# Kernel optimization log

Measured on AMD Instinct MI355X. Metric: run time of the kernel, lower is better.

Reference implementation:

```python
import jax, jax.numpy as jnp
import numpy as np

DIM = 512

def setup_inputs() -> dict:
    key = jax.random.key(0)
    k1, k2, k3 = jax.random.split(key, 3)
    context = jax.random.normal(k1, (64, 1024, DIM), dtype=jnp.float32)
    query = jax.random.normal(k2, (64, 128, DIM), dtype=jnp.float32)
    # nn.Linear(3*dim, 1, bias=False) weight, flattened to a (3*dim,) vector
    w0 = jax.random.normal(k3, (3 * DIM,), dtype=jnp.float32) * (1.0 / np.sqrt(3 * DIM))
    return {"context": context, "query": query, "w0": w0}

def reference(context, query, w0):
    # Trilinear similarity: sim[b,i,j] = w_c.c_i + w_q.q_j + w_m.(c_i*q_j)
    # (equivalent to Linear(concat([c, q, c*q])) without materializing the concat)
    d = context.shape[-1]
    wc, wq, wm = w0[:d], w0[d:2 * d], w0[2 * d:]
    sim = (context @ wc)[:, :, None] \
        + (query @ wq)[:, None, :] \
        + jnp.einsum('bid,bjd->bij', context * wm, query)  # (B, ctx, q)
    # Original: softmax over trailing dim of size 1 -> all ones (faithful to the bug)
    S = jnp.ones_like(sim)                 # (B, ctx, q)
    SS = jax.nn.softmax(sim, axis=1)       # softmax over context dim
    A = S @ query                          # (B, ctx, d)
    B = S @ jnp.swapaxes(SS, 1, 2) @ context  # (B, ctx, d)
    return (A, B)
```

## Files before the change

### kernel.cpp

```cpp
#include <hip/hip_runtime.h>
#include <hip/hip_bf16.h>

#define NB   64
#define NC   1024
#define NQ   128
#define DIMD 512
#define BK   64
#define NKC  (DIMD / BK)
#define LDK  (BK + 8)
#define TM   128
#define NTILE (NC / TM)

using short8  = __attribute__((ext_vector_type(8))) short;
using short4v = __attribute__((ext_vector_type(4))) short;
using f32x4   = __attribute__((ext_vector_type(4))) float;
typedef __fp16 half2v __attribute__((ext_vector_type(2)));

__device__ inline float dot4(float4 a, float4 b) {
    return a.x * b.x + a.y * b.y + a.z * b.z + a.w * b.w;
}

__global__ __launch_bounds__(256) void gemm_stats(
    const float* __restrict__ ctx, const float* __restrict__ qry,
    const float* __restrict__ w0, float* __restrict__ stats,
    unsigned short* __restrict__ simh)
{
    __shared__ __attribute__((aligned(16))) short As[TM][LDK];
    __shared__ __attribute__((aligned(16))) short Bs[NQ][LDK];
    __shared__ __attribute__((aligned(16))) float w0L[3 * DIMD];
    __shared__ float cwL[TM], qwL[NQ];
    __shared__ float sL[2][NQ];

    const int tid  = threadIdx.x;
    const int b    = blockIdx.x;
    const int bt   = blockIdx.y;
    const int i0   = bt * TM;
    const int w    = tid >> 6;
    const int lane = tid & 63;
    const int wr   = w >> 1, wcg = w & 1;
    const int RB   = wr * 64, CB = wcg * 64;
    const int n16  = lane & 15, qd = lane >> 4;

    for (int idx = tid; idx < 3 * DIMD; idx += 256) w0L[idx] = w0[idx];

    f32x4 acc[4][4];
#pragma unroll
    for (int ri = 0; ri < 4; ri++)
#pragma unroll
        for (int ci = 0; ci < 4; ci++)
#pragma unroll
            for (int e = 0; e < 4; e++) acc[ri][ci][e] = 0.f;

    const int col4  = n16 * 4;
    const int srow0 = w * 32 + qd;
    const float* cBase = ctx + ((size_t)(b * NC + i0 + srow0)) * DIMD + col4;
    const float* qBase = qry + ((size_t)(b * NQ + srow0)) * DIMD + col4;
    float cwp[8], qwp[8];
#pragma unroll
    for (int u = 0; u < 8; u++) { cwp[u] = 0.f; qwp[u] = 0.f; }

    for (int kc = 0; kc < NKC; kc++) {
        const int k0 = kc * BK;
        __syncthreads();
        float4 wcv = *(const float4*)&w0L[k0 + col4];
        float4 wqv = *(const float4*)&w0L[DIMD + k0 + col4];
        float4 wmv = *(const float4*)&w0L[2 * DIMD + k0 + col4];
#pragma unroll
        for (int u = 0; u < 8; u++) {
            const int row = w * 32 + u * 4 + qd;
            float4 v = *(const float4*)(cBase + k0 + (size_t)u * 4 * DIMD);
            cwp[u] += dot4(v, wcv);
            union { __hip_bfloat162 h[2]; short4v s; } pc;
            pc.h[0] = __float22bfloat162_rn(make_float2(v.x * wmv.x, v.y * wmv.y));
            pc.h[1] = __float22bfloat162_rn(make_float2(v.z * wmv.z, v.w * wmv.w));
            *(short4v*)&As[row][col4] = pc.s;

            float4 q = *(const float4*)(qBase + k0 + (size_t)u * 4 * DIMD);
            qwp[u] += dot4(q, wqv);
            union { __hip_bfloat162 h[2]; short4v s; } pq;
            pq.h[0] = __float22bfloat162_rn(make_float2(q.x, q.y));
            pq.h[1] = __float22bfloat162_rn(make_float2(q.z, q.w));
            *(short4v*)&Bs[row][col4] = pq.s;
        }
        __syncthreads();
#pragma unroll
        for (int ks = 0; ks < BK / 32; ks++) {
            const int kb = ks * 32 + qd * 8;
            short8 af[4], bfr[4];
#pragma unroll
            for (int ri = 0; ri < 4; ri++) af[ri] = *(const short8*)&As[RB + ri * 16 + n16][kb];
#pragma unroll
            for (int ci = 0; ci < 4; ci++) bfr[ci] = *(const short8*)&Bs[CB + ci * 16 + n16][kb];
#pragma unroll
            for (int ri = 0; ri < 4; ri++)
#pragma unroll
                for (int ci = 0; ci < 4; ci++)
                    acc[ri][ci] = __builtin_amdgcn_mfma_f32_16x16x32_bf16(
                        af[ri], bfr[ci], acc[ri][ci], 0, 0, 0);
        }
    }

#pragma unroll
    for (int u = 0; u < 8; u++) {
        float c = cwp[u], q = qwp[u];
#pragma unroll
        for (int off = 1; off < 16; off <<= 1) {
            c += __shfl_xor(c, off);
            q += __shfl_xor(q, off);
        }
        if (n16 == 0) {
            const int row = w * 32 + u * 4 + qd;
            cwL[row] = c; qwL[row] = q;
        }
    }
    __syncthreads();

#pragma unroll
    for (int ci = 0; ci < 4; ci++) {
        const int col = CB + ci * 16 + n16;
        const float qwv = qwL[col];
        unsigned short* simCol = simh + ((size_t)(b * NTILE + bt) * NQ + col) * TM;
        float s = 0.f;
#pragma unroll
        for (int ri = 0; ri < 4; ri++) {
            const int rbase = RB + ri * 16 + qd * 4;
            float v0 = acc[ri][ci][0] + cwL[rbase + 0] + qwv;
            float v1 = acc[ri][ci][1] + cwL[rbase + 1] + qwv;
            float v2 = acc[ri][ci][2] + cwL[rbase + 2] + qwv;
            float v3 = acc[ri][ci][3] + cwL[rbase + 3] + qwv;
            s += __expf(v0) + __expf(v1) + __expf(v2) + __expf(v3);
            half2v h01 = __builtin_amdgcn_cvt_pkrtz(v0, v1);
            half2v h23 = __builtin_amdgcn_cvt_pkrtz(v2, v3);
            uint2 pk;
            pk.x = __builtin_bit_cast(unsigned, h01);
            pk.y = __builtin_bit_cast(unsigned, h23);
            *(uint2*)&simCol[rbase] = pk;
        }
        s += __shfl_xor(s, 16);
        s += __shfl_xor(s, 32);
        if (qd == 0) sL[wr][col] = s;
    }
    __syncthreads();
    if (tid < NQ)
        stats[(size_t)(b * NTILE + bt) * NQ + tid] = sL[0][tid] + sL[1][tid];
}

__global__ void combine_stats(const float* __restrict__ stats, float* __restrict__ colstats)
{
    const int b = blockIdx.x, j = threadIdx.x;
    float s = 0.f;
    for (int t = 0; t < NTILE; t++)
        s += stats[(size_t)(b * NTILE + t) * NQ + j];
    colstats[(size_t)b * NQ + j] = 1.0f / s;
}

__global__ void arow_kernel(const float* __restrict__ qry, float* __restrict__ arow)
{
    const int b = blockIdx.x, h = blockIdx.y;
    const int d = h * 256 + threadIdx.x;
    float a = 0.f;
    const float* base = qry + (size_t)b * NQ * DIMD + d;
    for (int j = 0; j < NQ; j++) a += base[(size_t)j * DIMD];
    arow[(size_t)b * DIMD + d] = a;
}

__global__ __launch_bounds__(256) void rb_kernel(
    const float* __restrict__ ctx, const unsigned short* __restrict__ simh,
    const float* __restrict__ colstats, float* __restrict__ bpart)
{
    __shared__ __attribute__((aligned(16))) unsigned short simL[NQ * TM];
    __shared__ float izL[NQ];
    __shared__ float rpart[2][TM];
    __shared__ float rfin[TM];

    const int tid = threadIdx.x;
    const int b = blockIdx.x, bt = blockIdx.y;
    const int i0 = bt * TM;

    if (tid < NQ) izL[tid] = colstats[(size_t)b * NQ + tid];
    const unsigned short* tileSrc = simh + (size_t)(b * NTILE + bt) * NQ * TM;
#pragma unroll
    for (int it = 0; it < 8; it++) {
        const int idx = (tid + it * 256) * 8;
        *(uint4*)&simL[idx] = *(const uint4*)&tileSrc[idx];
    }
    __syncthreads();

    const int i = tid & 127, jh = tid >> 7;
    float r = 0.f;
    for (int j2 = 0; j2 < 64; j2++) {
        const int j = jh * 64 + j2;
        __fp16 hv = __builtin_bit_cast(__fp16, simL[j * TM + i]);
        r += __expf((float)hv) * izL[j];
    }
    rpart[jh][i] = r;
    __syncthreads();
    if (tid < TM) rfin[tid] = rpart[0][tid] + rpart[1][tid];
    __syncthreads();

    const int d0 = tid * 2;
    float bx = 0.f, by = 0.f;
    const float* cb2 = ctx + ((size_t)b * NC + i0) * DIMD + d0;
    for (int ii = 0; ii < TM; ii++) {
        float  rv = rfin[ii];
        float2 cv = *(const float2*)(cb2 + (size_t)ii * DIMD);
        bx += rv * cv.x; by += rv * cv.y;
    }
    float* bp = bpart + (size_t)(b * NTILE + bt) * DIMD + d0;
    bp[0] = bx; bp[1] = by;
}

__global__ void broadcast_out(const float* __restrict__ arow, const float* __restrict__ bpart,
                              float* __restrict__ out)
{
    const int b = blockIdx.x, ic = blockIdx.y;
    const int t = threadIdx.x;
    const int half = t >> 7;
    const int l = t & 127;
    const int d0 = l * 4;
    float4 val;
    if (half == 0) {
        val = *(const float4*)&arow[(size_t)b * DIMD + d0];
    } else {
        val.x = val.y = val.z = val.w = 0.f;
        for (int t8 = 0; t8 < NTILE; t8++) {
            float4 v = *(const float4*)&bpart[(size_t)(b * NTILE + t8) * DIMD + d0];
            val.x += v.x; val.y += v.y; val.z += v.z; val.w += v.w;
        }
    }
    size_t base = (size_t)half * ((size_t)NB * NC * DIMD)
                + ((size_t)b * NC + (size_t)ic * 32) * DIMD + d0;
    for (int i = 0; i < 32; i++)
        *(float4*)&out[base + (size_t)i * DIMD] = val;
}

extern "C" void kernel_launch(void* const* d_in, const int* in_sizes, int n_in,
                              void* d_out, int out_size, void* d_ws, size_t ws_size,
                              hipStream_t stream)
{
    const float* ctx = (const float*)d_in[0];
    const float* qry = (const float*)d_in[1];
    const float* w0  = (const float*)d_in[2];
    float* out = (float*)d_out;
    float* ws  = (float*)d_ws;

    float* stats    = ws;
    float* colstats = ws + 65536;
    float* arow     = ws + 73728;
    float* bpart    = ws + 106496;
    unsigned short* simh = (unsigned short*)(ws + 524288);

    arow_kernel<<<dim3(NB, 2), 256, 0, stream>>>(qry, arow);
    gemm_stats<<<dim3(NB, NTILE), 256, 0, stream>>>(ctx, qry, w0, stats, simh);
    combine_stats<<<NB, NQ, 0, stream>>>(stats, colstats);
    rb_kernel<<<dim3(NB, NTILE), 256, 0, stream>>>(ctx, simh, colstats, bpart);
    broadcast_out<<<dim3(NB, 32), 256, 0, stream>>>(arow, bpart, out);
}
```

Before: 432.1 us.

## Precompute bf16 operands and row dots in a prep kernel; async LDS loads in GEMM

Adds a prep kernel that converts context to bf16 and the weighted query to bf16, and computes the per-row context and query linear terms once. The GEMM then streams pre-converted bf16 tiles into swizzled LDS via global_load_lds and reads B fragments directly from global memory, removing in-loop conversion and weight application. The column-sum combine kernel is folded into rb_kernel, and rb_kernel reads bf16 context instead of fp32. This adds an extra pass over context and lowers the precision of the B output path.

```diff
diff --git a/kernel.cpp b/kernel.cpp
--- a/kernel.cpp
+++ b/kernel.cpp
@@ -7,29 +7,85 @@
 #define DIMD 512
 #define BK   64
 #define NKC  (DIMD / BK)
-#define LDK  (BK + 8)
 #define TM   128
 #define NTILE (NC / TM)
 
 using short8  = __attribute__((ext_vector_type(8))) short;
-using short4v = __attribute__((ext_vector_type(4))) short;
 using f32x4   = __attribute__((ext_vector_type(4))) float;
 typedef __fp16 half2v __attribute__((ext_vector_type(2)));
 
 __device__ inline float dot4(float4 a, float4 b) {
     return a.x * b.x + a.y * b.y + a.z * b.z + a.w * b.w;
 }
+__device__ inline float bf2f(unsigned short u) {
+    unsigned x = ((unsigned)u) << 16;
+    return __builtin_bit_cast(float, x);
+}
+__device__ inline ushort2 pkbf(float a, float b) {
+    union { __hip_bfloat162 h; ushort2 u; } x;
+    x.h = __float22bfloat162_rn(make_float2(a, b));
+    return x.u;
+}
+#define GLOAD_LDS16(g, l)                                             \
+    __builtin_amdgcn_global_load_lds(                                 \
+        (const __attribute__((address_space(1))) void*)(g),           \
+        (__attribute__((address_space(3))) void*)(l), 16, 0, 0)
+
+__global__ __launch_bounds__(256) void prep_kernel(
+    const float* __restrict__ ctx, const float* __restrict__ qry,
+    const float* __restrict__ w0,
+    unsigned short* __restrict__ C2, unsigned short* __restrict__ Q2,
+    float* __restrict__ cwG, float* __restrict__ qwG)
+{
+    const int wv   = blockIdx.x * 4 + (threadIdx.x >> 6);
+    const int lane = threadIdx.x & 63;
+    const int c0 = lane * 4, c1 = 256 + lane * 4;
+
+    if (wv < NB * NC) {
+        const float* src = ctx + (size_t)wv * DIMD;
+        float4 v0 = *(const float4*)(src + c0);
+        float4 v1 = *(const float4*)(src + c1);
+        float4 w0v = *(const float4*)(w0 + c0);
+        float4 w1v = *(const float4*)(w0 + c1);
+        float d = dot4(v0, w0v) + dot4(v1, w1v);
+#pragma unroll
+        for (int off = 1; off < 64; off <<= 1) d += __shfl_xor(d, off);
+        if (lane == 0) cwG[wv] = d;
+        ushort2 p0 = pkbf(v0.x, v0.y), p1 = pkbf(v0.z, v0.w);
+        ushort2 p2 = pkbf(v1.x, v1.y), p3 = pkbf(v1.z, v1.w);
+        union { ushort2 u2[2]; uint2 u; } a, bb;
+        a.u2[0] = p0; a.u2[1] = p1; bb.u2[0] = p2; bb.u2[1] = p3;
+        *(uint2*)&C2[(size_t)wv * DIMD + c0] = a.u;
+        *(uint2*)&C2[(size_t)wv * DIMD + c1] = bb.u;
+    } else {
+        const int r2 = wv - NB * NC;
+        const float* src = qry + (size_t)r2 * DIMD;
+        float4 v0 = *(const float4*)(src + c0);
+        float4 v1 = *(const float4*)(src + c1);
+        float4 wq0 = *(const float4*)(w0 + DIMD + c0);
+        float4 wq1 = *(const float4*)(w0 + DIMD + c1);
+        float4 wm0 = *(const float4*)(w0 + 2 * DIMD + c0);
+        float4 wm1 = *(const float4*)(w0 + 2 * DIMD + c1);
+        float d = dot4(v0, wq0) + dot4(v1, wq1);
+#pragma unroll
+        for (int off = 1; off < 64; off <<= 1) d += __shfl_xor(d, off);
+        if (lane == 0) qwG[r2] = d;
+        ushort2 p0 = pkbf(v0.x * wm0.x, v0.y * wm0.y), p1 = pkbf(v0.z * wm0.z, v0.w * wm0.w);
+        ushort2 p2 = pkbf(v1.x * wm1.x, v1.y * wm1.y), p3 = pkbf(v1.z * wm1.z, v1.w * wm1.w);
+        union { ushort2 u2[2]; uint2 u; } a, bb;
+        a.u2[0] = p0; a.u2[1] = p1; bb.u2[0] = p2; bb.u2[1] = p3;
+        *(uint2*)&Q2[(size_t)r2 * DIMD + c0] = a.u;
+        *(uint2*)&Q2[(size_t)r2 * DIMD + c1] = bb.u;
+    }
+}
 
 __global__ __launch_bounds__(256) void gemm_stats(
-    const float* __restrict__ ctx, const float* __restrict__ qry,
-    const float* __restrict__ w0, float* __restrict__ stats,
-    unsigned short* __restrict__ simh)
-{
-    __shared__ __attribute__((aligned(16))) short As[TM][LDK];
-    __shared__ __attribute__((aligned(16))) short Bs[NQ][LDK];
-    __shared__ __attribute__((aligned(16))) float w0L[3 * DIMD];
-    __shared__ float cwL[TM], qwL[NQ];
-    __shared__ float sL[2][NQ];
+    const unsigned short* __restrict__ C2, const unsigned short* __restrict__ Q2,
+    const float* __restrict__ cwG, const float* __restrict__ qwG,
+    float* __restrict__ stats, unsigned short* __restrict__ simh)
+{
+    __shared__ __attribute__((aligned(16))) unsigned short As[TM * BK];
+    __shared__ float cwL[TM], qwL[NQ], sL[2][NQ];
 
     const int tid  = threadIdx.x;
     const int b    = blockIdx.x;
@@ -41,7 +97,8 @@
     const int RB   = wr * 64, CB = wcg * 64;
     const int n16  = lane & 15, qd = lane >> 4;
 
-    for (int idx = tid; idx < 3 * DIMD; idx += 256) w0L[idx] = w0[idx];
+    if (tid < TM) cwL[tid] = cwG[b * NC + i0 + tid];
+    if (tid < NQ) qwL[tid] = qwG[b * NQ + tid];
 
     f32x4 acc[4][4];
 #pragma unroll
@@ -51,46 +108,30 @@
 #pragma unroll
             for (int e = 0; e < 4; e++) acc[ri][ci][e] = 0.f;
 
-    const int col4  = n16 * 4;
-    const int srow0 = w * 32 + qd;
-    const float* cBase = ctx + ((size_t)(b * NC + i0 + srow0)) * DIMD + col4;
-    const float* qBase = qry + ((size_t)(b * NQ + srow0)) * DIMD + col4;
-    float cwp[8], qwp[8];
-#pragma unroll
-    for (int u = 0; u < 8; u++) { cwp[u] = 0.f; qwp[u] = 0.f; }
+    const int a8 = lane >> 3, p8 = lane & 7;
+    const int kgd = p8 ^ (a8 & 7);
+    const unsigned short* gA = C2 + ((size_t)(b * NC + i0 + w * 32 + a8)) * DIMD + kgd * 8;
+    unsigned short* ldsA = &As[(w * 32) * BK];
+    const int sw = n16 & 7;
 
     for (int kc = 0; kc < NKC; kc++) {
         const int k0 = kc * BK;
         __syncthreads();
-        float4 wcv = *(const float4*)&w0L[k0 + col4];
-        float4 wqv = *(const float4*)&w0L[DIMD + k0 + col4];
-        float4 wmv = *(const float4*)&w0L[2 * DIMD + k0 + col4];
-#pragma unroll
-        for (int u = 0; u < 8; u++) {
-            const int row = w * 32 + u * 4 + qd;
-            float4 v = *(const float4*)(cBase + k0 + (size_t)u * 4 * DIMD);
-            cwp[u] += dot4(v, wcv);
-            union { __hip_bfloat162 h[2]; short4v s; } pc;
-            pc.h[0] = __float22bfloat162_rn(make_float2(v.x * wmv.x, v.y * wmv.y));
-            pc.h[1] = __float22bfloat162_rn(make_float2(v.z * wmv.z, v.w * wmv.w));
-            *(short4v*)&As[row][col4] = pc.s;
-
-            float4 q = *(const float4*)(qBase + k0 + (size_t)u * 4 * DIMD);
-            qwp[u] += dot4(q, wqv);
-            union { __hip_bfloat162 h[2]; short4v s; } pq;
-            pq.h[0] = __float22bfloat162_rn(make_float2(q.x, q.y));
-            pq.h[1] = __float22bfloat162_rn(make_float2(q.z, q.w));
-            *(short4v*)&Bs[row][col4] = pq.s;
-        }
+#pragma unroll
+        for (int u = 0; u < 4; u++)
+            GLOAD_LDS16(gA + k0 + (size_t)u * 8 * DIMD, ldsA + u * 8 * BK);
         __syncthreads();
 #pragma unroll
-        for (int ks = 0; ks < BK / 32; ks++) {
-            const int kb = ks * 32 + qd * 8;
+        for (int ks = 0; ks < 2; ks++) {
             short8 af[4], bfr[4];
 #pragma unroll
-            for (int ri = 0; ri < 4; ri++) af[ri] = *(const short8*)&As[RB + ri * 16 + n16][kb];
-#pragma unroll
-            for (int ci = 0; ci < 4; ci++) bfr[ci] = *(const short8*)&Bs[CB + ci * 16 + n16][kb];
+            for (int ci = 0; ci < 4; ci++)
+                bfr[ci] = *(const short8*)(Q2 + ((size_t)(b * NQ + CB + ci * 16 + n16)) * DIMD
+                                           + k0 + ks * 32 + qd * 8);
+#pragma unroll
+            for (int ri = 0; ri < 4; ri++)
+                af[ri] = *(const short8*)&As[(RB + ri * 16 + n16) * BK
+                                             + (((ks * 4 + qd) ^ sw) * 8)];
 #pragma unroll
             for (int ri = 0; ri < 4; ri++)
 #pragma unroll
@@ -99,21 +140,6 @@
                         af[ri], bfr[ci], acc[ri][ci], 0, 0, 0);
         }
     }
-
-#pragma unroll
-    for (int u = 0; u < 8; u++) {
-        float c = cwp[u], q = qwp[u];
-#pragma unroll
-        for (int off = 1; off < 16; off <<= 1) {
-            c += __shfl_xor(c, off);
-            q += __shfl_xor(q, off);
-        }
-        if (n16 == 0) {
-            const int row = w * 32 + u * 4 + qd;
-            cwL[row] = c; qwL[row] = q;
-        }
-    }
-    __syncthreads();
 
 #pragma unroll
     for (int ci = 0; ci < 4; ci++) {
@@ -145,15 +171,6 @@
         stats[(size_t)(b * NTILE + bt) * NQ + tid] = sL[0][tid] + sL[1][tid];
 }
 
-__global__ void combine_stats(const float* __restrict__ stats, float* __restrict__ colstats)
-{
-    const int b = blockIdx.x, j = threadIdx.x;
-    float s = 0.f;
-    for (int t = 0; t < NTILE; t++)
-        s += stats[(size_t)(b * NTILE + t) * NQ + j];
-    colstats[(size_t)b * NQ + j] = 1.0f / s;
-}
-
 __global__ void arow_kernel(const float* __restrict__ qry, float* __restrict__ arow)
 {
     const int b = blockIdx.x, h = blockIdx.y;
@@ -165,8 +182,8 @@
 }
 
 __global__ __launch_bounds__(256) void rb_kernel(
-    const float* __restrict__ ctx, const unsigned short* __restrict__ simh,
-    const float* __restrict__ colstats, float* __restrict__ bpart)
+    const unsigned short* __restrict__ C2, const unsigned short* __restrict__ simh,
+    const float* __restrict__ stats, float* __restrict__ bpart)
 {
     __shared__ __attribute__((aligned(16))) unsigned short simL[NQ * TM];
     __shared__ float izL[NQ];
@@ -177,7 +194,12 @@
     const int b = blockIdx.x, bt = blockIdx.y;
     const int i0 = bt * TM;
 
-    if (tid < NQ) izL[tid] = colstats[(size_t)b * NQ + tid];
+    if (tid < NQ) {
+        float s = 0.f;
+        for (int t = 0; t < NTILE; t++)
+            s += stats[(size_t)(b * NTILE + t) * NQ + tid];
+        izL[tid] = 1.0f / s;
+    }
     const unsigned short* tileSrc = simh + (size_t)(b * NTILE + bt) * NQ * TM;
 #pragma unroll
     for (int it = 0; it < 8; it++) {
@@ -200,11 +222,11 @@
 
     const int d0 = tid * 2;
     float bx = 0.f, by = 0.f;
-    const float* cb2 = ctx + ((size_t)b * NC + i0) * DIMD + d0;
+    const unsigned short* cb2 = C2 + ((size_t)(b * NC + i0)) * DIMD + d0;
     for (int ii = 0; ii < TM; ii++) {
-        float  rv = rfin[ii];
-        float2 cv = *(const float2*)(cb2 + (size_t)ii * DIMD);
-        bx += rv * cv.x; by += rv * cv.y;
+        float rv = rfin[ii];
+        ushort2 cv = *(const ushort2*)(cb2 + (size_t)ii * DIMD);
+        bx += rv * bf2f(cv.x); by += rv * bf2f(cv.y);
     }
     float* bp = bpart + (size_t)(b * NTILE + bt) * DIMD + d0;
     bp[0] = bx; bp[1] = by;
@@ -242,17 +264,20 @@
     const float* qry = (const float*)d_in[1];
     const float* w0  = (const float*)d_in[2];
     float* out = (float*)d_out;
-    float* ws  = (float*)d_ws;
-
-    float* stats    = ws;
-    float* colstats = ws + 65536;
-    float* arow     = ws + 73728;
-    float* bpart    = ws + 106496;
-    unsigned short* simh = (unsigned short*)(ws + 524288);
-
+    char*  ws  = (char*)d_ws;
+
+    float* stats = (float*)(ws);
+    float* arow  = (float*)(ws + (1u << 20));
+    float* bpart = (float*)(ws + (2u << 20));
+    float* cwG   = (float*)(ws + (4u << 20));
+    float* qwG   = (float*)(ws + (5u << 20));
+    unsigned short* simh = (unsigned short*)(ws + (8u << 20));
+    unsigned short* C2   = (unsigned short*)(ws + (32u << 20));
+    unsigned short* Q2   = (unsigned short*)(ws + (104u << 20));
+
+    prep_kernel<<<18432, 256, 0, stream>>>(ctx, qry, w0, C2, Q2, cwG, qwG);
     arow_kernel<<<dim3(NB, 2), 256, 0, stream>>>(qry, arow);
-    gemm_stats<<<dim3(NB, NTILE), 256, 0, stream>>>(ctx, qry, w0, stats, simh);
-    combine_stats<<<NB, NQ, 0, stream>>>(stats, colstats);
-    rb_kernel<<<dim3(NB, NTILE), 256, 0, stream>>>(ctx, simh, colstats, bpart);
+    gemm_stats<<<dim3(NB, NTILE), 256, 0, stream>>>(C2, Q2, cwG, qwG, stats, simh);
+    rb_kernel<<<dim3(NB, NTILE), 256, 0, stream>>>(C2, simh, stats, bpart);
     broadcast_out<<<dim3(NB, 32), 256, 0, stream>>>(arow, bpart, out);
 }
```

Measured after the change: 432.1 us. About the same (+0.0%).

## Fuse column softmax into GEMM by tiling over query columns, drop sim buffer

Applied to the files above, without the earlier changes.

The GEMM is restructured so each block owns 16 query columns across all 1024 context rows. This lets the column softmax normalisation and the row-sum reduction happen in registers, with no fp16 similarity matrix written out and no separate stats-combine pass. The arow reduction is folded into a new brow kernel that also computes the context weighted sum, cutting five launches to three. The trade-off is that context is re-read from global memory by eight blocks per batch (one per query group) and converted to bf16 on the fly. This raises context traffic and reduces per-block MFMA reuse.

```diff
diff --git a/kernel.cpp b/kernel.cpp
--- a/kernel.cpp
+++ b/kernel.cpp
@@ -7,210 +7,187 @@
 #define DIMD 512
 #define BK   64
 #define NKC  (DIMD / BK)
-#define LDK  (BK + 8)
-#define TM   128
-#define NTILE (NC / TM)
+#define LDKB (BK + 8)
 
 using short8  = __attribute__((ext_vector_type(8))) short;
 using short4v = __attribute__((ext_vector_type(4))) short;
 using f32x4   = __attribute__((ext_vector_type(4))) float;
-typedef __fp16 half2v __attribute__((ext_vector_type(2)));
 
 __device__ inline float dot4(float4 a, float4 b) {
     return a.x * b.x + a.y * b.y + a.z * b.z + a.w * b.w;
 }
-
-__global__ __launch_bounds__(256) void gemm_stats(
+__device__ inline short4v pk4(float a, float b, float c, float d) {
+    union { __hip_bfloat162 h[2]; short4v s; } x;
+    x.h[0] = __float22bfloat162_rn(make_float2(a, b));
+    x.h[1] = __float22bfloat162_rn(make_float2(c, d));
+    return x.s;
+}
+
+__global__ __launch_bounds__(256) void colgemm_kernel(
     const float* __restrict__ ctx, const float* __restrict__ qry,
-    const float* __restrict__ w0, float* __restrict__ stats,
-    unsigned short* __restrict__ simh)
-{
-    __shared__ __attribute__((aligned(16))) short As[TM][LDK];
-    __shared__ __attribute__((aligned(16))) short Bs[NQ][LDK];
+    const float* __restrict__ w0, float* __restrict__ rpart)
+{
+    __shared__ __attribute__((aligned(16))) short Bs[16][LDKB];
     __shared__ __attribute__((aligned(16))) float w0L[3 * DIMD];
-    __shared__ float cwL[TM], qwL[NQ];
-    __shared__ float sL[2][NQ];
+    __shared__ float cwL[NC];
+    __shared__ float qwL[16];
+    __shared__ float zL[4][16];
 
     const int tid  = threadIdx.x;
     const int b    = blockIdx.x;
-    const int bt   = blockIdx.y;
-    const int i0   = bt * TM;
+    const int jg   = blockIdx.y;
     const int w    = tid >> 6;
     const int lane = tid & 63;
-    const int wr   = w >> 1, wcg = w & 1;
-    const int RB   = wr * 64, CB = wcg * 64;
     const int n16  = lane & 15, qd = lane >> 4;
 
     for (int idx = tid; idx < 3 * DIMD; idx += 256) w0L[idx] = w0[idx];
 
-    f32x4 acc[4][4];
-#pragma unroll
-    for (int ri = 0; ri < 4; ri++)
-#pragma unroll
-        for (int ci = 0; ci < 4; ci++)
-#pragma unroll
-            for (int e = 0; e < 4; e++) acc[ri][ci][e] = 0.f;
-
-    const int col4  = n16 * 4;
-    const int srow0 = w * 32 + qd;
-    const float* cBase = ctx + ((size_t)(b * NC + i0 + srow0)) * DIMD + col4;
-    const float* qBase = qry + ((size_t)(b * NQ + srow0)) * DIMD + col4;
-    float cwp[8], qwp[8];
-#pragma unroll
-    for (int u = 0; u < 8; u++) { cwp[u] = 0.f; qwp[u] = 0.f; }
+    f32x4 acc[16];
+#pragma unroll
+    for (int rt = 0; rt < 16; rt++)
+#pragma unroll
+        for (int e = 0; e < 4; e++) acc[rt][e] = 0.f;
+
+    const int brow = tid >> 4, bk4 = (tid & 15) * 4;
+    const float* qRow = qry + ((size_t)(b * NQ + jg * 16 + brow)) * DIMD + bk4;
+    float qwp = 0.f;
+
+    const float* cBase = ctx + ((size_t)(b * NC + w * 256 + n16)) * DIMD + qd * 8;
+    float cwp[16];
+#pragma unroll
+    for (int rt = 0; rt < 16; rt++) cwp[rt] = 0.f;
+
+    __syncthreads();
 
     for (int kc = 0; kc < NKC; kc++) {
         const int k0 = kc * BK;
+        {
+            float4 q  = *(const float4*)(qRow + k0);
+            float4 wq = *(const float4*)&w0L[DIMD + k0 + bk4];
+            float4 wm = *(const float4*)&w0L[2 * DIMD + k0 + bk4];
+            qwp += dot4(q, wq);
+            *(short4v*)&Bs[brow][bk4] = pk4(q.x * wm.x, q.y * wm.y, q.z * wm.z, q.w * wm.w);
+        }
         __syncthreads();
-        float4 wcv = *(const float4*)&w0L[k0 + col4];
-        float4 wqv = *(const float4*)&w0L[DIMD + k0 + col4];
-        float4 wmv = *(const float4*)&w0L[2 * DIMD + k0 + col4];
-#pragma unroll
-        for (int u = 0; u < 8; u++) {
-            const int row = w * 32 + u * 4 + qd;
-            float4 v = *(const float4*)(cBase + k0 + (size_t)u * 4 * DIMD);
-            cwp[u] += dot4(v, wcv);
-            union { __hip_bfloat162 h[2]; short4v s; } pc;
-            pc.h[0] = __float22bfloat162_rn(make_float2(v.x * wmv.x, v.y * wmv.y));
-            pc.h[1] = __float22bfloat162_rn(make_float2(v.z * wmv.z, v.w * wmv.w));
-            *(short4v*)&As[row][col4] = pc.s;
-
-            float4 q = *(const float4*)(qBase + k0 + (size_t)u * 4 * DIMD);
-            qwp[u] += dot4(q, wqv);
-            union { __hip_bfloat162 h[2]; short4v s; } pq;
-            pq.h[0] = __float22bfloat162_rn(make_float2(q.x, q.y));
-            pq.h[1] = __float22bfloat162_rn(make_float2(q.z, q.w));
-            *(short4v*)&Bs[row][col4] = pq.s;
+#pragma unroll
+        for (int ks = 0; ks < 2; ks++) {
+            const int kw = k0 + ks * 32 + qd * 8;
+            float4 wc0 = *(const float4*)&w0L[kw];
+            float4 wc1 = *(const float4*)&w0L[kw + 4];
+            short8 bfr = *(const short8*)&Bs[n16][ks * 32 + qd * 8];
+#pragma unroll
+            for (int rt = 0; rt < 16; rt++) {
+                const float* ap = cBase + (size_t)rt * 16 * DIMD + k0 + ks * 32;
+                float4 a0 = *(const float4*)(ap);
+                float4 a1 = *(const float4*)(ap + 4);
+                cwp[rt] += dot4(a0, wc0) + dot4(a1, wc1);
+                union { short4v s4[2]; short8 s8; } af;
+                af.s4[0] = pk4(a0.x, a0.y, a0.z, a0.w);
+                af.s4[1] = pk4(a1.x, a1.y, a1.z, a1.w);
+                acc[rt] = __builtin_amdgcn_mfma_f32_16x16x32_bf16(af.s8, bfr, acc[rt], 0, 0, 0);
+            }
         }
         __syncthreads();
-#pragma unroll
-        for (int ks = 0; ks < BK / 32; ks++) {
-            const int kb = ks * 32 + qd * 8;
-            short8 af[4], bfr[4];
-#pragma unroll
-            for (int ri = 0; ri < 4; ri++) af[ri] = *(const short8*)&As[RB + ri * 16 + n16][kb];
-#pragma unroll
-            for (int ci = 0; ci < 4; ci++) bfr[ci] = *(const short8*)&Bs[CB + ci * 16 + n16][kb];
-#pragma unroll
-            for (int ri = 0; ri < 4; ri++)
-#pragma unroll
-                for (int ci = 0; ci < 4; ci++)
-                    acc[ri][ci] = __builtin_amdgcn_mfma_f32_16x16x32_bf16(
-                        af[ri], bfr[ci], acc[ri][ci], 0, 0, 0);
-        }
-    }
-
-#pragma unroll
-    for (int u = 0; u < 8; u++) {
-        float c = cwp[u], q = qwp[u];
-#pragma unroll
-        for (int off = 1; off < 16; off <<= 1) {
-            c += __shfl_xor(c, off);
-            q += __shfl_xor(q, off);
-        }
-        if (n16 == 0) {
-            const int row = w * 32 + u * 4 + qd;
-            cwL[row] = c; qwL[row] = q;
-        }
-    }
-    __syncthreads();
-
-#pragma unroll
-    for (int ci = 0; ci < 4; ci++) {
-        const int col = CB + ci * 16 + n16;
-        const float qwv = qwL[col];
-        unsigned short* simCol = simh + ((size_t)(b * NTILE + bt) * NQ + col) * TM;
+    }
+
+    {
+        float q = qwp;
+#pragma unroll
+        for (int off = 1; off < 16; off <<= 1) q += __shfl_xor(q, off);
+        if ((tid & 15) == 0 && w == (brow >> 2)) qwL[brow] = q;
+    }
+#pragma unroll
+    for (int rt = 0; rt < 16; rt++) {
+        float c = cwp[rt];
+        c += __shfl_xor(c, 16);
+        c += __shfl_xor(c, 32);
+        if (qd == 0) cwL[w * 256 + rt * 16 + n16] = c;
+    }
+    __syncthreads();
+
+    const float qwv = qwL[n16];
+    float zp = 0.f;
+#pragma unroll
+    for (int rt = 0; rt < 16; rt++) {
+        const int rbase = w * 256 + rt * 16 + qd * 4;
+#pragma unroll
+        for (int rg = 0; rg < 4; rg++) {
+            float e = __expf(acc[rt][rg] + cwL[rbase + rg] + qwv);
+            acc[rt][rg] = e;
+            zp += e;
+        }
+    }
+    zp += __shfl_xor(zp, 16);
+    zp += __shfl_xor(zp, 32);
+    if (qd == 0) zL[w][n16] = zp;
+    __syncthreads();
+    const float iz = 1.0f / (zL[0][n16] + zL[1][n16] + zL[2][n16] + zL[3][n16]);
+
+    float* rp = rpart + ((size_t)(b * 8 + jg)) * NC;
+#pragma unroll
+    for (int rt = 0; rt < 16; rt++) {
+        f32x4 rv;
+#pragma unroll
+        for (int rg = 0; rg < 4; rg++) {
+            float v = acc[rt][rg] * iz;
+#pragma unroll
+            for (int off = 1; off < 16; off <<= 1) v += __shfl_xor(v, off);
+            rv[rg] = v;
+        }
+        if (n16 == 0)
+            *(f32x4*)&rp[w * 256 + rt * 16 + qd * 4] = rv;
+    }
+}
+
+__global__ __launch_bounds__(256) void brow_kernel(
+    const float* __restrict__ ctx, const float* __restrict__ qry,
+    const float* __restrict__ rpart, float* __restrict__ browG,
+    float* __restrict__ arowG)
+{
+    __shared__ float rfullL[NC];
+    __shared__ float bredL[4][64];
+    __shared__ float aredL[4][64];
+
+    const int tid = threadIdx.x;
+    const int b = blockIdx.x, dg = blockIdx.y;
+
+#pragma unroll
+    for (int g = 0; g < 4; g++) {
+        const int i = g * 256 + tid;
         float s = 0.f;
 #pragma unroll
-        for (int ri = 0; ri < 4; ri++) {
-            const int rbase = RB + ri * 16 + qd * 4;
-            float v0 = acc[ri][ci][0] + cwL[rbase + 0] + qwv;
-            float v1 = acc[ri][ci][1] + cwL[rbase + 1] + qwv;
-            float v2 = acc[ri][ci][2] + cwL[rbase + 2] + qwv;
-            float v3 = acc[ri][ci][3] + cwL[rbase + 3] + qwv;
-            s += __expf(v0) + __expf(v1) + __expf(v2) + __expf(v3);
-            half2v h01 = __builtin_amdgcn_cvt_pkrtz(v0, v1);
-            half2v h23 = __builtin_amdgcn_cvt_pkrtz(v2, v3);
-            uint2 pk;
-            pk.x = __builtin_bit_cast(unsigned, h01);
-            pk.y = __builtin_bit_cast(unsigned, h23);
-            *(uint2*)&simCol[rbase] = pk;
-        }
-        s += __shfl_xor(s, 16);
-        s += __shfl_xor(s, 32);
-        if (qd == 0) sL[wr][col] = s;
-    }
-    __syncthreads();
-    if (tid < NQ)
-        stats[(size_t)(b * NTILE + bt) * NQ + tid] = sL[0][tid] + sL[1][tid];
-}
-
-__global__ void combine_stats(const float* __restrict__ stats, float* __restrict__ colstats)
-{
-    const int b = blockIdx.x, j = threadIdx.x;
-    float s = 0.f;
-    for (int t = 0; t < NTILE; t++)
-        s += stats[(size_t)(b * NTILE + t) * NQ + j];
-    colstats[(size_t)b * NQ + j] = 1.0f / s;
-}
-
-__global__ void arow_kernel(const float* __restrict__ qry, float* __restrict__ arow)
-{
-    const int b = blockIdx.x, h = blockIdx.y;
-    const int d = h * 256 + threadIdx.x;
-    float a = 0.f;
-    const float* base = qry + (size_t)b * NQ * DIMD + d;
-    for (int j = 0; j < NQ; j++) a += base[(size_t)j * DIMD];
-    arow[(size_t)b * DIMD + d] = a;
-}
-
-__global__ __launch_bounds__(256) void rb_kernel(
-    const float* __restrict__ ctx, const unsigned short* __restrict__ simh,
-    const float* __restrict__ colstats, float* __restrict__ bpart)
-{
-    __shared__ __attribute__((aligned(16))) unsigned short simL[NQ * TM];
-    __shared__ float izL[NQ];
-    __shared__ float rpart[2][TM];
-    __shared__ float rfin[TM];
-
-    const int tid = threadIdx.x;
-    const int b = blockIdx.x, bt = blockIdx.y;
-    const int i0 = bt * TM;
-
-    if (tid < NQ) izL[tid] = colstats[(size_t)b * NQ + tid];
-    const unsigned short* tileSrc = simh + (size_t)(b * NTILE + bt) * NQ * TM;
-#pragma unroll
-    for (int it = 0; it < 8; it++) {
-        const int idx = (tid + it * 256) * 8;
-        *(uint4*)&simL[idx] = *(const uint4*)&tileSrc[idx];
-    }
-    __syncthreads();
-
-    const int i = tid & 127, jh = tid >> 7;
-    float r = 0.f;
-    for (int j2 = 0; j2 < 64; j2++) {
-        const int j = jh * 64 + j2;
-        __fp16 hv = __builtin_bit_cast(__fp16, simL[j * TM + i]);
-        r += __expf((float)hv) * izL[j];
-    }
-    rpart[jh][i] = r;
-    __syncthreads();
-    if (tid < TM) rfin[tid] = rpart[0][tid] + rpart[1][tid];
-    __syncthreads();
-
-    const int d0 = tid * 2;
-    float bx = 0.f, by = 0.f;
-    const float* cb2 = ctx + ((size_t)b * NC + i0) * DIMD + d0;
-    for (int ii = 0; ii < TM; ii++) {
-        float  rv = rfin[ii];
-        float2 cv = *(const float2*)(cb2 + (size_t)ii * DIMD);
-        bx += rv * cv.x; by += rv * cv.y;
-    }
-    float* bp = bpart + (size_t)(b * NTILE + bt) * DIMD + d0;
-    bp[0] = bx; bp[1] = by;
-}
-
-__global__ void broadcast_out(const float* __restrict__ arow, const float* __restrict__ bpart,
+        for (int t = 0; t < 8; t++)
+            s += rpart[((size_t)(b * 8 + t)) * NC + i];
+        rfullL[i] = s;
+    }
+    __syncthreads();
+
+    const int d = dg * 64 + (tid & 63);
+    const int g = tid >> 6;
+    {
+        float s = 0.f;
+        const float* cb = ctx + ((size_t)(b * NC + g * 256)) * DIMD + d;
+        for (int ii = 0; ii < 256; ii++)
+            s += rfullL[g * 256 + ii] * cb[(size_t)ii * DIMD];
+        bredL[g][tid & 63] = s;
+    }
+    {
+        float s = 0.f;
+        const float* qb = qry + ((size_t)(b * NQ + g * 32)) * DIMD + d;
+        for (int j = 0; j < 32; j++)
+            s += qb[(size_t)j * DIMD];
+        aredL[g][tid & 63] = s;
+    }
+    __syncthreads();
+    if (tid < 64) {
+        browG[(size_t)b * DIMD + dg * 64 + tid] =
+            bredL[0][tid] + bredL[1][tid] + bredL[2][tid] + bredL[3][tid];
+        arowG[(size_t)b * DIMD + dg * 64 + tid] =
+            aredL[0][tid] + aredL[1][tid] + aredL[2][tid] + aredL[3][tid];
+    }
+}
+
+__global__ void broadcast_out(const float* __restrict__ arowG, const float* __restrict__ browG,
                               float* __restrict__ out)
 {
     const int b = blockIdx.x, ic = blockIdx.y;
@@ -219,15 +196,8 @@
     const int l = t & 127;
     const int d0 = l * 4;
     float4 val;
-    if (half == 0) {
-        val = *(const float4*)&arow[(size_t)b * DIMD + d0];
-    } else {
-        val.x = val.y = val.z = val.w = 0.f;
-        for (int t8 = 0; t8 < NTILE; t8++) {
-            float4 v = *(const float4*)&bpart[(size_t)(b * NTILE + t8) * DIMD + d0];
-            val.x += v.x; val.y += v.y; val.z += v.z; val.w += v.w;
-        }
-    }
+    if (half == 0) val = *(const float4*)&arowG[(size_t)b * DIMD + d0];
+    else           val = *(const float4*)&browG[(size_t)b * DIMD + d0];
     size_t base = (size_t)half * ((size_t)NB * NC * DIMD)
                 + ((size_t)b * NC + (size_t)ic * 32) * DIMD + d0;
     for (int i = 0; i < 32; i++)
@@ -242,17 +212,13 @@
     const float* qry = (const float*)d_in[1];
     const float* w0  = (const float*)d_in[2];
     float* out = (float*)d_out;
-    float* ws  = (float*)d_ws;
-
-    float* stats    = ws;
-    float* colstats = ws + 65536;
-    float* arow     = ws + 73728;
-    float* bpart    = ws + 106496;
-    unsigned short* simh = (unsigned short*)(ws + 524288);
-
-    arow_kernel<<<dim3(NB, 2), 256, 0, stream>>>(qry, arow);
-    gemm_stats<<<dim3(NB, NTILE), 256, 0, stream>>>(ctx, qry, w0, stats, simh);
-    combine_stats<<<NB, NQ, 0, stream>>>(stats, colstats);
-    rb_kernel<<<dim3(NB, NTILE), 256, 0, stream>>>(ctx, simh, colstats, bpart);
-    broadcast_out<<<dim3(NB, 32), 256, 0, stream>>>(arow, bpart, out);
-}
+    char*  ws  = (char*)d_ws;
+
+    float* rpart = (float*)(ws);
+    float* browG = (float*)(ws + (4u << 20));
+    float* arowG = (float*)(ws + (5u << 20));
+
+    colgemm_kernel<<<dim3(NB, 8), 256, 0, stream>>>(ctx, qry, w0, rpart);
+    brow_kernel<<<dim3(NB, 8), 256, 0, stream>>>(ctx, qry, rpart, browG, arowG);
+    broadcast_out<<<dim3(NB, 32), 256, 0, stream>>>(arowG, browG, out);
+}
```

After: 483.9 us. 12.0% more time.

## Load context A-fragments directly from global, fold wm into query, fuse small kernels

Applied to the files above, without the earlier changes.

The GEMM kernel no longer stages context through LDS. Each wave loads its A fragments straight from global memory and converts them to bf16. The wm weight is now applied to the query operand, stored in a swizzled LDS layout, and the context·wc dot product is computed by an extra MFMA against a wc row appended to the B tile. The combine_stats and arow kernels are folded into rb_kernel, which removes two launches, but this costs uncoalesced direct global A loads and some bf16 precision on the wc projection.

```diff
diff --git a/kernel.cpp b/kernel.cpp
--- a/kernel.cpp
+++ b/kernel.cpp
@@ -7,9 +7,9 @@
 #define DIMD 512
 #define BK   64
 #define NKC  (DIMD / BK)
-#define LDK  (BK + 8)
 #define TM   128
 #define NTILE (NC / TM)
+#define BROWS 144
 
 using short8  = __attribute__((ext_vector_type(8))) short;
 using short4v = __attribute__((ext_vector_type(4))) short;
@@ -19,17 +19,23 @@
 __device__ inline float dot4(float4 a, float4 b) {
     return a.x * b.x + a.y * b.y + a.z * b.z + a.w * b.w;
 }
+__device__ inline short8 pk8(float4 a, float4 b) {
+    union { __hip_bfloat162 h[4]; short8 s; } x;
+    x.h[0] = __float22bfloat162_rn(make_float2(a.x, a.y));
+    x.h[1] = __float22bfloat162_rn(make_float2(a.z, a.w));
+    x.h[2] = __float22bfloat162_rn(make_float2(b.x, b.y));
+    x.h[3] = __float22bfloat162_rn(make_float2(b.z, b.w));
+    return x.s;
+}
 
 __global__ __launch_bounds__(256) void gemm_stats(
     const float* __restrict__ ctx, const float* __restrict__ qry,
     const float* __restrict__ w0, float* __restrict__ stats,
     unsigned short* __restrict__ simh)
 {
-    __shared__ __attribute__((aligned(16))) short As[TM][LDK];
-    __shared__ __attribute__((aligned(16))) short Bs[NQ][LDK];
+    __shared__ __attribute__((aligned(16))) short Bs[BROWS * BK];
     __shared__ __attribute__((aligned(16))) float w0L[3 * DIMD];
-    __shared__ float cwL[TM], qwL[NQ];
-    __shared__ float sL[2][NQ];
+    __shared__ float cwL[TM], qwL[NQ], sL[2][NQ];
 
     const int tid  = threadIdx.x;
     const int b    = blockIdx.x;
@@ -42,76 +48,100 @@
     const int n16  = lane & 15, qd = lane >> 4;
 
     for (int idx = tid; idx < 3 * DIMD; idx += 256) w0L[idx] = w0[idx];
-
-    f32x4 acc[4][4];
+    for (int idx = tid; idx < (BROWS - 129) * BK / 2; idx += 256)
+        ((unsigned*)&Bs[129 * BK])[idx] = 0u;
+
+    f32x4 acc[4][4], cwacc[4];
+#pragma unroll
+    for (int ri = 0; ri < 4; ri++) {
+#pragma unroll
+        for (int ci = 0; ci < 4; ci++)
+#pragma unroll
+            for (int e = 0; e < 4; e++) acc[ri][ci][e] = 0.f;
+#pragma unroll
+        for (int e = 0; e < 4; e++) cwacc[ri][e] = 0.f;
+    }
+
+    const int srow = tid >> 3, kg = tid & 7;
+    float qwp[4] = {0.f, 0.f, 0.f, 0.f};
+
+    const float* aBase[4];
 #pragma unroll
     for (int ri = 0; ri < 4; ri++)
-#pragma unroll
-        for (int ci = 0; ci < 4; ci++)
-#pragma unroll
-            for (int e = 0; e < 4; e++) acc[ri][ci][e] = 0.f;
-
-    const int col4  = n16 * 4;
-    const int srow0 = w * 32 + qd;
-    const float* cBase = ctx + ((size_t)(b * NC + i0 + srow0)) * DIMD + col4;
-    const float* qBase = qry + ((size_t)(b * NQ + srow0)) * DIMD + col4;
-    float cwp[8], qwp[8];
-#pragma unroll
-    for (int u = 0; u < 8; u++) { cwp[u] = 0.f; qwp[u] = 0.f; }
+        aBase[ri] = ctx + ((size_t)(b * NC + i0 + RB + ri * 16 + n16)) * DIMD + qd * 8;
 
     for (int kc = 0; kc < NKC; kc++) {
         const int k0 = kc * BK;
         __syncthreads();
-        float4 wcv = *(const float4*)&w0L[k0 + col4];
-        float4 wqv = *(const float4*)&w0L[DIMD + k0 + col4];
-        float4 wmv = *(const float4*)&w0L[2 * DIMD + k0 + col4];
-#pragma unroll
-        for (int u = 0; u < 8; u++) {
-            const int row = w * 32 + u * 4 + qd;
-            float4 v = *(const float4*)(cBase + k0 + (size_t)u * 4 * DIMD);
-            cwp[u] += dot4(v, wcv);
-            union { __hip_bfloat162 h[2]; short4v s; } pc;
-            pc.h[0] = __float22bfloat162_rn(make_float2(v.x * wmv.x, v.y * wmv.y));
-            pc.h[1] = __float22bfloat162_rn(make_float2(v.z * wmv.z, v.w * wmv.w));
-            *(short4v*)&As[row][col4] = pc.s;
-
-            float4 q = *(const float4*)(qBase + k0 + (size_t)u * 4 * DIMD);
-            qwp[u] += dot4(q, wqv);
-            union { __hip_bfloat162 h[2]; short4v s; } pq;
-            pq.h[0] = __float22bfloat162_rn(make_float2(q.x, q.y));
-            pq.h[1] = __float22bfloat162_rn(make_float2(q.z, q.w));
-            *(short4v*)&Bs[row][col4] = pq.s;
+#pragma unroll
+        for (int it = 0; it < 4; it++) {
+            const int row = it * 32 + srow;
+            const int col = k0 + kg * 8;
+            float4 q0 = *(const float4*)(qry + ((size_t)(b * NQ + row)) * DIMD + col);
+            float4 q1 = *(const float4*)(qry + ((size_t)(b * NQ + row)) * DIMD + col + 4);
+            float4 wq0 = *(const float4*)&w0L[DIMD + col];
+            float4 wq1 = *(const float4*)&w0L[DIMD + col + 4];
+            float4 wm0 = *(const float4*)&w0L[2 * DIMD + col];
+            float4 wm1 = *(const float4*)&w0L[2 * DIMD + col + 4];
+            qwp[it] += dot4(q0, wq0) + dot4(q1, wq1);
+            float4 m0, m1;
+            m0.x = q0.x * wm0.x; m0.y = q0.y * wm0.y; m0.z = q0.z * wm0.z; m0.w = q0.w * wm0.w;
+            m1.x = q1.x * wm1.x; m1.y = q1.y * wm1.y; m1.z = q1.z * wm1.z; m1.w = q1.w * wm1.w;
+            *(short8*)&Bs[row * BK + ((kg ^ (row & 7)) * 8)] = pk8(m0, m1);
+        }
+        if (tid < 8) {
+            const int col = k0 + tid * 8;
+            float4 c0 = *(const float4*)&w0L[col];
+            float4 c1 = *(const float4*)&w0L[col + 4];
+            *(short8*)&Bs[128 * BK + (tid * 8)] = pk8(c0, c1);
         }
         __syncthreads();
 #pragma unroll
-        for (int ks = 0; ks < BK / 32; ks++) {
-            const int kb = ks * 32 + qd * 8;
+        for (int ks = 0; ks < 2; ks++) {
+            const int g = ks * 4 + qd;
             short8 af[4], bfr[4];
 #pragma unroll
-            for (int ri = 0; ri < 4; ri++) af[ri] = *(const short8*)&As[RB + ri * 16 + n16][kb];
-#pragma unroll
-            for (int ci = 0; ci < 4; ci++) bfr[ci] = *(const short8*)&Bs[CB + ci * 16 + n16][kb];
+            for (int ri = 0; ri < 4; ri++) {
+                const float* ap = aBase[ri] + k0 + ks * 32;
+                float4 a0 = *(const float4*)(ap);
+                float4 a1 = *(const float4*)(ap + 4);
+                af[ri] = pk8(a0, a1);
+            }
+#pragma unroll
+            for (int ci = 0; ci < 4; ci++) {
+                const int rowb = CB + ci * 16 + n16;
+                bfr[ci] = *(const short8*)&Bs[rowb * BK + ((g ^ (rowb & 7)) * 8)];
+            }
 #pragma unroll
             for (int ri = 0; ri < 4; ri++)
 #pragma unroll
                 for (int ci = 0; ci < 4; ci++)
                     acc[ri][ci] = __builtin_amdgcn_mfma_f32_16x16x32_bf16(
                         af[ri], bfr[ci], acc[ri][ci], 0, 0, 0);
-        }
-    }
-
-#pragma unroll
-    for (int u = 0; u < 8; u++) {
-        float c = cwp[u], q = qwp[u];
-#pragma unroll
-        for (int off = 1; off < 16; off <<= 1) {
-            c += __shfl_xor(c, off);
-            q += __shfl_xor(q, off);
-        }
-        if (n16 == 0) {
-            const int row = w * 32 + u * 4 + qd;
-            cwL[row] = c; qwL[row] = q;
-        }
+            if (wcg == 0) {
+                const int rowb = 128 + n16;
+                short8 bcw = *(const short8*)&Bs[rowb * BK + ((g ^ (rowb & 7)) * 8)];
+#pragma unroll
+                for (int ri = 0; ri < 4; ri++)
+                    cwacc[ri] = __builtin_amdgcn_mfma_f32_16x16x32_bf16(
+                        af[ri], bcw, cwacc[ri], 0, 0, 0);
+            }
+        }
+    }
+
+#pragma unroll
+    for (int it = 0; it < 4; it++) {
+        float q = qwp[it];
+#pragma unroll
+        for (int off = 1; off < 8; off <<= 1) q += __shfl_xor(q, off);
+        if ((tid & 7) == 0) qwL[it * 32 + srow] = q;
+    }
+    if (wcg == 0 && n16 == 0) {
+#pragma unroll
+        for (int ri = 0; ri < 4; ri++)
+#pragma unroll
+            for (int rg = 0; rg < 4; rg++)
+                cwL[RB + ri * 16 + qd * 4 + rg] = cwacc[ri][rg];
     }
     __syncthreads();
 
@@ -145,28 +175,10 @@
         stats[(size_t)(b * NTILE + bt) * NQ + tid] = sL[0][tid] + sL[1][tid];
 }
 
-__global__ void combine_stats(const float* __restrict__ stats, float* __restrict__ colstats)
-{
-    const int b = blockIdx.x, j = threadIdx.x;
-    float s = 0.f;
-    for (int t = 0; t < NTILE; t++)
-        s += stats[(size_t)(b * NTILE + t) * NQ + j];
-    colstats[(size_t)b * NQ + j] = 1.0f / s;
-}
-
-__global__ void arow_kernel(const float* __restrict__ qry, float* __restrict__ arow)
-{
-    const int b = blockIdx.x, h = blockIdx.y;
-    const int d = h * 256 + threadIdx.x;
-    float a = 0.f;
-    const float* base = qry + (size_t)b * NQ * DIMD + d;
-    for (int j = 0; j < NQ; j++) a += base[(size_t)j * DIMD];
-    arow[(size_t)b * DIMD + d] = a;
-}
-
 __global__ __launch_bounds__(256) void rb_kernel(
-    const float* __restrict__ ctx, const unsigned short* __restrict__ simh,
-    const float* __restrict__ colstats, float* __restrict__ bpart)
+    const float* __restrict__ ctx, const float* __restrict__ qry,
+    const unsigned short* __restrict__ simh, const float* __restrict__ stats,
+    float* __restrict__ bpart, float* __restrict__ arow)
 {
     __shared__ __attribute__((aligned(16))) unsigned short simL[NQ * TM];
     __shared__ float izL[NQ];
@@ -177,7 +189,12 @@
     const int b = blockIdx.x, bt = blockIdx.y;
     const int i0 = bt * TM;
 
-    if (tid < NQ) izL[tid] = colstats[(size_t)b * NQ + tid];
+    if (tid < NQ) {
+        float s = 0.f;
+        for (int t = 0; t < NTILE; t++)
+            s += stats[(size_t)(b * NTILE + t) * NQ + tid];
+        izL[tid] = 1.0f / s;
+    }
     const unsigned short* tileSrc = simh + (size_t)(b * NTILE + bt) * NQ * TM;
 #pragma unroll
     for (int it = 0; it < 8; it++) {
@@ -199,15 +216,27 @@
     __syncthreads();
 
     const int d0 = tid * 2;
-    float bx = 0.f, by = 0.f;
-    const float* cb2 = ctx + ((size_t)b * NC + i0) * DIMD + d0;
-    for (int ii = 0; ii < TM; ii++) {
-        float  rv = rfin[ii];
-        float2 cv = *(const float2*)(cb2 + (size_t)ii * DIMD);
-        bx += rv * cv.x; by += rv * cv.y;
-    }
-    float* bp = bpart + (size_t)(b * NTILE + bt) * DIMD + d0;
-    bp[0] = bx; bp[1] = by;
+    {
+        float bx = 0.f, by = 0.f;
+        const float* cb2 = ctx + ((size_t)(b * NC + i0)) * DIMD + d0;
+        for (int ii = 0; ii < TM; ii++) {
+            float  rv = rfin[ii];
+            float2 cv = *(const float2*)(cb2 + (size_t)ii * DIMD);
+            bx += rv * cv.x; by += rv * cv.y;
+        }
+        float* bp = bpart + (size_t)(b * NTILE + bt) * DIMD + d0;
+        bp[0] = bx; bp[1] = by;
+    }
+    if (bt == 0) {
+        float ax = 0.f, ay = 0.f;
+        const float* qb = qry + (size_t)b * NQ * DIMD + d0;
+        for (int j = 0; j < NQ; j++) {
+            float2 v = *(const float2*)(qb + (size_t)j * DIMD);
+            ax += v.x; ay += v.y;
+        }
+        float2 rr; rr.x = ax; rr.y = ay;
+        *(float2*)&arow[(size_t)b * DIMD + d0] = rr;
+    }
 }
 
 __global__ void broadcast_out(const float* __restrict__ arow, const float* __restrict__ bpart,
@@ -242,17 +271,14 @@
     const float* qry = (const float*)d_in[1];
     const float* w0  = (const float*)d_in[2];
     float* out = (float*)d_out;
-    float* ws  = (float*)d_ws;
-
-    float* stats    = ws;
-    float* colstats = ws + 65536;
-    float* arow     = ws + 73728;
-    float* bpart    = ws + 106496;
-    unsigned short* simh = (unsigned short*)(ws + 524288);
-
-    arow_kernel<<<dim3(NB, 2), 256, 0, stream>>>(qry, arow);
+    char*  ws  = (char*)d_ws;
+
+    float* stats = (float*)(ws);
+    float* bpart = (float*)(ws + (1u << 20));
+    float* arow  = (float*)(ws + (3u << 20));
+    unsigned short* simh = (unsigned short*)(ws + (8u << 20));
+
     gemm_stats<<<dim3(NB, NTILE), 256, 0, stream>>>(ctx, qry, w0, stats, simh);
-    combine_stats<<<NB, NQ, 0, stream>>>(stats, colstats);
-    rb_kernel<<<dim3(NB, NTILE), 256, 0, stream>>>(ctx, simh, colstats, bpart);
+    rb_kernel<<<dim3(NB, NTILE), 256, 0, stream>>>(ctx, qry, simh, stats, bpart, arow);
     broadcast_out<<<dim3(NB, 32), 256, 0, stream>>>(arow, bpart, out);
 }
```

Result: slower. 449.8 us (+4.1%).
